# Optimization experiments

Hardware: AMD Instinct MI355X
Metric: run time of the kernel (lower is better)

Reference implementation:

```python
import jax, jax.numpy as jnp
import numpy as np

B, T, N, D = 32, 12, 325, 64
H = 4           # geo_num_heads == t_num_heads
HD = D // H     # head_dim = 16
M_SP = 32       # spatial frequency modes (min(32, N//2))
M_T = T // 2    # temporal frequency modes (all low modes)
SCALE = HD ** -0.5


def _lin(x, W):
    # torch nn.Linear (no bias): y = x @ W.T, W: [out, in]
    return jnp.einsum('btnd,ed->btne', x, W)


def _spatial(x, Wq, Wk, Wv, weights_Q, sp_modes):
    # FEDformer-style frequency attention over the node axis N
    q, k, v = _lin(x, Wq), _lin(x, Wk), _lin(x, Wv)          # [B,T,N,D]
    prep = lambda y: y.reshape(B, T, N, H, HD).transpose(0, 1, 3, 4, 2)  # [B,T,H,HD,N]
    qn = prep(q) / jnp.linalg.norm(q)   # global Frobenius norm (torch.norm with no dim)
    kn = prep(k) / jnp.linalg.norm(k)
    vn = prep(v)
    # rfft over nodes, gather selected modes (scatter-into-zeros in torch == gather here
    # since target indices are 0..M-1)
    qf = jnp.fft.rfft(qn, axis=-1)[..., sp_modes]            # [B,T,H,HD,M] c64
    kf = jnp.fft.rfft(kn, axis=-1)[..., sp_modes]
    vf = jnp.fft.rfft(vn, axis=-1)[..., sp_modes]
    M = M_SP
    qg = qf.transpose(0, 1, 2, 4, 3)[:, :, :, :, None, :]    # [B,T,H,M,1,HD]
    wq = jnp.broadcast_to(weights_Q.astype(jnp.complex64), (B, T, H, M, M - 1, HD))
    q_cat = jnp.concatenate([qg, wq], axis=4)                # [B,T,H,M,M,HD]
    kg = kf.transpose(0, 1, 2, 4, 3)[:, :, :, None, :, :]    # [B,T,H,1,M,HD]
    att = kg * jnp.conj(q_cat) * SCALE                       # [B,T,H,M,M,HD] c64
    att = jax.nn.softmax(jnp.abs(att), axis=-2).astype(jnp.complex64)
    att = att.transpose(0, 1, 2, 3, 5, 4)                    # [B,T,H,M,HD,M]
    vg = vf[:, :, :, None, :, :]                             # [B,T,H,1,HD,M]
    out = (vg * jnp.conj(att)).mean(axis=3)                  # [B,T,H,HD,M]
    out_ft = jnp.zeros((B, T, H, HD, N // 2 + 1), jnp.complex64).at[..., sp_modes].set(out)
    y = jnp.fft.irfft(out_ft, n=N, axis=-1)                  # [B,T,H,HD,N]
    return y.transpose(0, 1, 4, 2, 3).reshape(B, T, N, D)


def _temporal(x, Wq, Wk, Wv, weights_Q_t, t_modes):
    # frequency attention over the time axis T with causal (tril) mask.
    # NOTE: torch reshapes the [B,T,N,D] buffer directly as [B,N,T,H,HD] (raw view),
    # so we replicate that exact buffer reinterpretation.
    q, k, v = _lin(x, Wq), _lin(x, Wk), _lin(x, Wv)
    prep = lambda y: y.reshape(B, N, T, H, HD).transpose(0, 1, 3, 4, 2)  # [B,N,H,HD,T]
    qn = prep(q); kn = prep(k); vn = prep(v)
    qn = qn / jnp.linalg.norm(qn)
    kn = kn / jnp.linalg.norm(kn)
    qf = jnp.fft.rfft(qn, axis=-1)[..., t_modes]             # [B,N,H,HD,Mt]
    kf = jnp.fft.rfft(kn, axis=-1)[..., t_modes]
    vf = jnp.fft.rfft(vn, axis=-1)[..., t_modes]
    Mt = M_T
    qg = qf.transpose(0, 1, 2, 4, 3)[:, :, :, :, None, :]    # [B,N,H,Mt,1,HD]
    wq = jnp.broadcast_to(weights_Q_t.astype(jnp.complex64), (B, N, H, Mt, Mt - 1, HD))
    q_cat = jnp.concatenate([qg, wq], axis=4)                # [B,N,H,Mt,Mt,HD]
    kg = kf.transpose(0, 1, 2, 4, 3)[:, :, :, :, None, :]    # [B,N,H,Mt,1,HD] (unsqueeze(4) in torch)
    att = kg * jnp.conj(q_cat) * SCALE                       # [B,N,H,Mt,Mt,HD]
    att = att.transpose(0, 1, 2, 5, 3, 4)                    # [B,N,H,HD,Mt,Mt]
    mask = jnp.tril(jnp.ones((Mt, Mt), jnp.float32))
    att = att * mask                                         # zero above diagonal
    attw = jax.nn.softmax(jnp.abs(att), axis=-1).astype(jnp.complex64)
    vg = vf[..., None]                                       # [B,N,H,HD,Mt,1]
    out = (vg * jnp.conj(attw)).mean(axis=-1)                # [B,N,H,HD,Mt]
    out_ft = jnp.zeros((B, N, H, HD, T // 2 + 1), jnp.complex64).at[..., t_modes].set(out)
    y = jnp.fft.irfft(out_ft, n=T, axis=-1)                  # [B,N,H,HD,T]
    return y.transpose(0, 4, 1, 2, 3).reshape(B, T, N, D)


def _gcn(x, adj, W_fc1, W_mlp, b_mlp):
    a = adj / jnp.sum(adj, axis=1, keepdims=True)            # row-normalized
    agg = jnp.einsum('btkd,nk->btnd', x, a)
    h = jnp.einsum('btnd,ed->btne', agg, W_fc1)              # fc1 (no bias)
    return jnp.einsum('btnd,ed->btne', h, W_mlp) + b_mlp     # mlp (bias)


def _forward(x, adj, Wq_geo, Wk_geo, Wv_geo, Wq_t, Wk_t, Wv_t,
             W_fc1, W_mlp, b_mlp, weights_Q, weights_Q_t, sp_modes, t_modes):
    gcn_out = _gcn(x, adj, W_fc1, W_mlp, b_mlp)
    sp_x = _spatial(x, Wq_geo, Wk_geo, Wv_geo, weights_Q, sp_modes)
    te_x = _temporal(x, Wq_t, Wk_t, Wv_t, weights_Q_t, t_modes)
    return gcn_out + sp_x + te_x   # proj_drop is identity (p=0)


def setup_inputs() -> dict:
    key = jax.random.key(0)
    ks = jax.random.split(key, 13)
    w = lambda k, s: jax.random.normal(k, s, dtype=jnp.float32) * 0.05
    rng = np.random.default_rng(0)
    sp_modes = np.sort(rng.permutation(N // 2)[:M_SP]).astype(np.int32)
    t_modes = np.arange(M_T, dtype=np.int32)  # modes_T == T//2 selects all low modes
    return {
        'x': jax.random.normal(ks[0], (B, T, N, D), dtype=jnp.float32),
        'adj': jax.random.uniform(ks[1], (N, N), dtype=jnp.float32),
        'Wq_geo': w(ks[2], (D, D)), 'Wk_geo': w(ks[3], (D, D)), 'Wv_geo': w(ks[4], (D, D)),
        'Wq_t': w(ks[5], (D, D)), 'Wk_t': w(ks[6], (D, D)), 'Wv_t': w(ks[7], (D, D)),
        'W_fc1': w(ks[8], (D, D)), 'W_mlp': w(ks[9], (D, D)), 'b_mlp': w(ks[10], (D,)),
        'weights_Q': jax.random.normal(ks[11], (M_SP, M_SP - 1, HD), dtype=jnp.float32),
        'weights_Q_t': jax.random.normal(ks[12], (M_T, M_T - 1, HD), dtype=jnp.float32),
        'sp_modes': jnp.asarray(sp_modes),
        't_modes': jnp.asarray(t_modes),
    }


def reference(x, adj, Wq_geo, Wk_geo, Wv_geo, Wq_t, Wk_t, Wv_t,
              W_fc1, W_mlp, b_mlp, weights_Q, weights_Q_t, sp_modes, t_modes):
    return _forward(x, adj, Wq_geo, Wk_geo, Wv_geo, Wq_t, Wk_t, Wv_t,
                    W_fc1, W_mlp, b_mlp, weights_Q, weights_Q_t, sp_modes, t_modes)
```

## Files before the change

### kernel.cpp

```cpp
#include <hip/hip_runtime.h>


typedef unsigned short u16;
typedef short short8 __attribute__((ext_vector_type(8)));
typedef float floatx4 __attribute__((ext_vector_type(4)));

__device__ __forceinline__ u16 f2bf(float f) {
  union { float fp; unsigned int u; } v; v.fp = f;
  unsigned int x = v.u;
  x += 0x7FFF + ((x >> 16) & 1);
  return (u16)(x >> 16);
}

constexpr size_t OFF_NPART = 4096;
constexpr size_t OFF_WQA  = 8208;
constexpr size_t OFF_ANB  = 24080;
constexpr size_t OFF_TB   = 81280;
constexpr size_t OFF_WVTB = 92544;
constexpr size_t OFF_WBB  = 94592;
constexpr size_t OFF_T2   = 102080;
constexpr size_t OFF_OFT  = 112480;
constexpr size_t OFF_XCT  = 898912;
constexpr size_t OFF_XA   = 13211488;
constexpr size_t OFF_WSPB = OFF_XA + 8192;

__global__ __launch_bounds__(256) void k_prep(const float* __restrict__ adj,
                                              const float* __restrict__ Wmlp,
                                              const float* __restrict__ Wfc1,
                                              const float* __restrict__ wQ,
                                              const float* __restrict__ Wvt,
                                              const float* __restrict__ Wq,
                                              const float* __restrict__ Wk,
                                              const float* __restrict__ Wv,
                                              const int* __restrict__ sp_modes,
                                              float* __restrict__ ws) {
  __shared__ float red[256];
  const int tid = threadIdx.x;
  const int blk = blockIdx.x;
  u16* WBBu = (u16*)(ws + OFF_WBB);
  if (blk == 0) {
    for (int o = tid; o < 4096; o += 256) {
      int g = o >> 6, dd = o & 63;
      float s = 0.f;
      for (int e = 0; e < 64; ++e)
        s = fmaf(Wmlp[g * 64 + e], Wfc1[e * 64 + dd], s);
      WBBu[o] = f2bf(s);
    }
  } else if (blk < 9) {
    for (int i = (blk - 1) * 256 + tid; i < 15872; i += 2048)
      ws[OFF_WQA + i] = fabsf(wQ[i]);
  } else if (blk < 334) {
    const int n = blk - 9;
    float p = 0.f;
    for (int k = tid; k < 325; k += 256) p += adj[n * 325 + k];
    red[tid] = p;
    __syncthreads();
    for (int s2 = 128; s2 > 0; s2 >>= 1) {
      if (tid < s2) red[tid] += red[tid + s2];
      __syncthreads();
    }
    const float inv = 1.f / red[0];
    u16* ANB = (u16*)(ws + OFF_ANB);
    for (int k = tid; k < 352; k += 256)
      ANB[(size_t)n * 352 + k] = (k < 325) ? f2bf(adj[n * 325 + k] * inv) : (u16)0;
  } else if (blk < 366) {
    const int j = blk - 334;
    const int f = sp_modes[j];
    const float wgt = (f == 0) ? 1.f : 2.f;
    u16* T2B = (u16*)(ws + OFF_T2);
    u16* TB = (u16*)(ws + OFF_TB);
    const int row_re = 8 * (j >> 2) + (j & 3);
    const int row_im = row_re + 4;
    for (int n = tid; n < 352; n += 256) {
      float c = 0.f, s = 0.f;
      if (n < 325) {
        int mm = (f * n) % 325;
        float th = 6.283185307179586f * (float)mm * (1.f / 325.f);
        c = cosf(th);
        s = sinf(th);
      }
      TB[(size_t)row_re * 352 + n] = f2bf(c);
      TB[(size_t)row_im * 352 + n] = f2bf(-s);
      if (n < 325) {
        T2B[(size_t)n * 64 + 2 * j] = f2bf(wgt * (1.f / 325.f) * c);
        T2B[(size_t)n * 64 + 2 * j + 1] = f2bf(-wgt * (1.f / 325.f) * s);
      }
    }
  } else if (blk == 366) {
    for (int i = tid; i < 8192; i += 256) {
      const int r = i >> 6, e = i & 63;
      const float* src = (r < 64) ? Wq : Wk;
      WBBu[4096 + i] = f2bf(src[(size_t)(r & 63) * 64 + e]);
    }
  } else if (blk == 367) {
    u16* WSPBu = (u16*)(ws + OFF_WSPB);
    for (int i = tid; i < 12288; i += 256) {
      const int r = i >> 6, e = i & 63;
      const float* src = (r < 64) ? Wq : (r < 128) ? Wk : Wv;
      WSPBu[i] = f2bf(src[(size_t)(r & 63) * 64 + e]);
    }
  } else if (blk == 368) {
    u16* WVTBu = (u16*)(ws + OFF_WVTB);
    for (int i = tid; i < 4096; i += 256) WVTBu[i] = f2bf(Wvt[i]);
  } else {
    const int idx = (blk - 369) * 256 + tid;
    u16* p = (u16*)(ws + OFF_XCT) + (size_t)(idx >> 6) * 22528 + (size_t)(idx & 63) * 352;
    for (int c = 325; c < 352; ++c) p[c] = 0;
  }
}

__global__ __launch_bounds__(512, 3) void k_linear2(const float* __restrict__ x,
                                                    float* __restrict__ ws) {
  __shared__ __align__(16) u16 XA[128 * 72];
  __shared__ float reds[16];
  const int tid = threadIdx.x;
  const int wv = tid >> 6, lane = tid & 63, lc = lane & 15, quad = lane >> 4;
  const size_t base = (size_t)blockIdx.x * 128;
  const u16* WBBu = (const u16*)(ws + OFF_WBB);

  for (int i = tid; i < 2048; i += 512) {
    const int row = i >> 4, e0 = (i & 15) * 4;
    const float4 v = *(const float4*)(x + (base + row) * 64 + e0);
    u16* dst = &XA[row * 72 + e0];
    dst[0] = f2bf(v.x); dst[1] = f2bf(v.y); dst[2] = f2bf(v.z); dst[3] = f2bf(v.w);
  }
  __syncthreads();

  floatx4 acc[12] = {};
#pragma unroll
  for (int kc = 0; kc < 2; ++kc) {
    const short8 af = *(const short8*)&XA[(16 * wv + lc) * 72 + kc * 32 + quad * 8];
#pragma unroll
    for (int ni = 0; ni < 12; ++ni) {
      const short8 bf_ = *(const short8*)&WBBu[(ni * 16 + lc) * 64 + kc * 32 + quad * 8];
      acc[ni] = __builtin_amdgcn_mfma_f32_16x16x32_bf16(af, bf_, acc[ni], 0, 0, 0);
    }
  }

  float sq = 0.f, sk = 0.f;
#pragma unroll
  for (int reg = 0; reg < 4; ++reg) {
#pragma unroll
    for (int ni = 0; ni < 4; ++ni) {
      const float v = acc[4 + ni][reg];
      sq = fmaf(v, v, sq);
    }
#pragma unroll
    for (int ni = 0; ni < 4; ++ni) {
      const float v = acc[8 + ni][reg];
      sk = fmaf(v, v, sk);
    }
  }
  for (int off = 32; off > 0; off >>= 1) {
    sq += __shfl_down(sq, off);
    sk += __shfl_down(sk, off);
  }
  if (lane == 0) { reds[wv] = sq; reds[8 + wv] = sk; }
  __syncthreads();
  if (tid == 0) {
    const float a = reds[0] + reds[1] + reds[2] + reds[3] +
                    reds[4] + reds[5] + reds[6] + reds[7];
    const float b = reds[8] + reds[9] + reds[10] + reds[11] +
                    reds[12] + reds[13] + reds[14] + reds[15];
    *(float2*)(ws + OFF_NPART + 2 * (size_t)blockIdx.x) = make_float2(a, b);
  }

  u16* xcT = XA;
#pragma unroll
  for (int ni = 0; ni < 4; ++ni)
#pragma unroll
    for (int reg = 0; reg < 4; ++reg)
      xcT[(ni * 16 + lc) * 132 + 16 * wv + quad * 4 + reg] = f2bf(acc[ni][reg]);
  __syncthreads();
  u16* XCT = (u16*)(ws + OFF_XCT);
  for (int i = tid; i < 8192; i += 512) {
    const int d = i >> 7, r = i & 127;
    const unsigned int row = (unsigned int)(base + r);
    const unsigned int bt = row / 325u;
    const unsigned int n = row - bt * 325u;
    XCT[(size_t)bt * 22528 + (size_t)d * 352 + n] = xcT[d * 132 + r];
  }
}

__global__ __launch_bounds__(256) void k_spatial3(const float* __restrict__ x,
                                                  float* __restrict__ ws) {
  __shared__ __align__(16) float smem[12816];
  const int tid = threadIdx.x;
  const int bt = blockIdx.x;
  const int lane = tid & 63, wv = tid >> 6;
  const int lc = lane & 15, quad = lane >> 4;
  u16* XBu = (u16*)smem;

  {
    float psq = 0.f, psk = 0.f;
    for (int p = tid; p < 975; p += 256) {
      const float2 v = *(const float2*)(ws + OFF_NPART + 2 * (size_t)p);
      psq += v.x; psk += v.y;
    }
    for (int off = 32; off > 0; off >>= 1) {
      psq += __shfl_down(psq, off);
      psk += __shfl_down(psk, off);
    }
    if (lane == 0) { smem[12800 + wv] = psq; smem[12808 + wv] = psk; }
  }

  const u16* TB = (const u16*)(ws + OFF_TB);
  const u16* WSPBu = (const u16*)(ws + OFF_WSPB);
  const float* xb = x + (size_t)bt * 20800;
  const int br = tid & 31, be0 = (tid >> 5) * 8;

  {
    float va[4][8];
#pragma unroll
    for (int g = 0; g < 3; ++g) {
      const int nkc = (g < 2) ? 4 : 3;
#pragma unroll
      for (int u = 0; u < 4; ++u) {
        if (u >= nkc) break;
        const int k0 = (g * 4 + u) * 32;
        if (k0 + br < 325) {
          const float* src = xb + (size_t)(k0 + br) * 64 + be0;
          *(float4*)&va[u][0] = *(const float4*)src;
          *(float4*)&va[u][4] = *(const float4*)(src + 4);
        } else {
#pragma unroll
          for (int w = 0; w < 8; ++w) va[u][w] = 0.f;
        }
      }
#pragma unroll
      for (int u = 0; u < 4; ++u) {
        if (u >= nkc) break;
        const int k0 = (g * 4 + u) * 32;
#pragma unroll
        for (int w = 0; w < 8; ++w)
          XBu[(be0 + w) * 360 + k0 + br] = f2bf(va[u][w]);
      }
    }
  }
  __syncthreads();

  floatx4 accA[4] = {};
#pragma unroll
  for (int kc = 0; kc < 11; ++kc) {
    const short8 af = *(const short8*)&TB[(size_t)(16 * wv + lc) * 352 + kc * 32 + quad * 8];
#pragma unroll
    for (int t = 0; t < 4; ++t) {
      const short8 bf_ = *(const short8*)&XBu[(t * 16 + lc) * 360 + kc * 32 + quad * 8];
      accA[t] = __builtin_amdgcn_mfma_f32_16x16x32_bf16(af, bf_, accA[t], 0, 0, 0);
    }
  }
  __syncthreads();

  u16* xfl2 = XBu;
#pragma unroll
  for (int t = 0; t < 4; ++t)
#pragma unroll
    for (int r = 0; r < 4; ++r)
      xfl2[(t >> 1) * 2560 + (16 * wv + quad * 4 + r) * 40 + (t & 1) * 16 + lc] =
          f2bf(accA[t][r]);
  __syncthreads();

  floatx4 acc2[12] = {};
#pragma unroll
  for (int kc2 = 0; kc2 < 2; ++kc2) {
    const short8 af2 = *(const short8*)&xfl2[kc2 * 2560 + (16 * wv + lc) * 40 + quad * 8];
#pragma unroll
    for (int t = 0; t < 12; ++t) {
      const short8 bf2 = *(const short8*)&WSPBu[(t * 16 + lc) * 64 + kc2 * 32 + quad * 8];
      acc2[t] = __builtin_amdgcn_mfma_f32_16x16x32_bf16(af2, bf2, acc2[t], 0, 0, 0);
    }
  }
  __syncthreads();

  float* sq_q = smem + 2560;
  float* sq_k = smem + 4608;
  float* vfre = smem + 6656;
  float* vfim = smem + 8704;
  float* wbar = smem + 10752;
  for (int i = tid; i < 2048; i += 256) wbar[i] = 0.f;
  {
    const int fb = 8 * wv + ((quad >= 2) ? 4 : 0);
    const int isim = quad & 1;
#pragma unroll
    for (int t = 0; t < 12; ++t) {
      const int mat = t >> 2;
      const int d = (t & 3) * 16 + lc;
#pragma unroll
      for (int r = 0; r < 4; ++r) {
        const float v = acc2[t][r];
        if (mat == 2) {
          if (isim) vfim[(fb + r) * 64 + d] = v;
          else vfre[(fb + r) * 64 + d] = v;
        } else {
          const float s2 = v * v + __shfl_xor(v * v, 16);
          if (!isim) {
            if (mat == 0) sq_q[(fb + r) * 64 + d] = s2;
            else sq_k[(fb + r) * 64 + d] = s2;
          }
        }
      }
    }
  }
  __syncthreads();
  float nqs = 0.f, nks = 0.f;
#pragma unroll
  for (int w = 0; w < 4; ++w) { nqs += smem[12800 + w]; nks += smem[12808 + w]; }
  const float inv_nq = rsqrtf(nqs);
  const float inv_nk = rsqrtf(nks);
  for (int i = tid; i < 2048; i += 256)
    sq_k[i] = 0.25f * inv_nk * sqrtf(sq_k[i]);
  __syncthreads();
  {
    const int d = tid & 63, fb2 = tid >> 6, hd = d & 15;
    const float* wqa = ws + OFF_WQA;
    float wacc[32];
#pragma unroll
    for (int j = 0; j < 32; ++j) wacc[j] = 0.f;
    for (int r8 = 0; r8 < 8; ++r8) {
      const int m = fb2 + (r8 << 2);
      const float aq = inv_nq * sqrtf(sq_q[m * 64 + d]);
      float sv[32];
      float mx = -1e30f;
#pragma unroll
      for (int j = 0; j < 32; ++j) {
        const float a = (j == 0) ? aq : wqa[(m * 31 + (j - 1)) * 16 + hd];
        const float s = sq_k[j * 64 + d] * a;
        sv[j] = s;
        mx = fmaxf(mx, s);
      }
      float sum = 0.f;
#pragma unroll
      for (int j = 0; j < 32; ++j) {
        const float ev = __expf(sv[j] - mx);
        sv[j] = ev;
        sum += ev;
      }
      const float sc = 0.03125f / sum;
#pragma unroll
      for (int j = 0; j < 32; ++j) wacc[j] += sv[j] * sc;
    }
#pragma unroll
    for (int j = 0; j < 32; ++j) atomicAdd(&wbar[j * 64 + d], wacc[j]);
  }
  __syncthreads();
  unsigned int* OFTu = (unsigned int*)(ws + OFF_OFT) + (size_t)bt * 2048;
  for (int i2 = tid; i2 < 2048; i2 += 256) {
    const int d = i2 >> 5, j = i2 & 31;
    const float w = wbar[j * 64 + d];
    const unsigned int lo = f2bf(vfre[j * 64 + d] * w);
    const unsigned int hi = f2bf(vfim[j * 64 + d] * w);
    OFTu[i2] = lo | (hi << 16);
  }
}

__global__ __launch_bounds__(256) void k_xa(const float* __restrict__ x,
                                            float* __restrict__ ws) {
  const int idx = blockIdx.x * 256 + threadIdx.x;
  if (idx >= 32 * 325 * 16) return;
  const int dq = idx & 15;
  const int n = (idx >> 4) % 325;
  const int b = idx / (16 * 325);
  const float* xp = x + ((size_t)b * 3900 + (size_t)n * 12) * 64 + dq * 4;
  float4 s = make_float4(0.f, 0.f, 0.f, 0.f);
  float sign = 1.f;
  for (int k = 0; k < 12; ++k) {
    const float4 v = *(const float4*)(xp + (size_t)k * 64);
    s.x += sign * v.x; s.y += sign * v.y; s.z += sign * v.z; s.w += sign * v.w;
    sign = -sign;
  }
  *(float4*)(ws + OFF_XA + ((size_t)b * 325 + n) * 64 + dq * 4) = s;
}

__global__ __launch_bounds__(256) void k_final2(const float* __restrict__ x,
                                                const float* __restrict__ bmlp,
                                                float* __restrict__ ws,
                                                float* __restrict__ out) {
  const int tid = threadIdx.x;
  const int bt = blockIdx.x / 3, mc = blockIdx.x % 3;
  const int m0 = mc * 128;
  const int wave = tid >> 6, lane = tid & 63;
  const int quad = lane >> 4, lc = lane & 15;

  const u16* ANB = (const u16*)(ws + OFF_ANB);
  const u16* T2B = (const u16*)(ws + OFF_T2);
  const u16* XCT = (const u16*)(ws + OFF_XCT) + (size_t)bt * 22528;
  const u16* OFT = (const u16*)(ws + OFF_OFT) + (size_t)bt * 4096;
  const u16* WVTBu = (const u16*)(ws + OFF_WVTB);

  const int b = bt / 12, t = bt - b * 12;
  const float sgn12 = ((t & 1) ? -1.f : 1.f) * (1.f / 12.f);

  floatx4 acc[2][4] = {};

#pragma unroll
  for (int c13 = 0; c13 < 13; ++c13) {
    const bool gcn = (c13 < 11);
    const u16* Asrc = gcn ? ANB : T2B;
    const int astr = gcn ? 352 : 64;
    const int acol = gcn ? c13 * 32 : (c13 - 11) * 32;
    const u16* Bsrc = gcn ? XCT : OFT;
    const int bstr = gcn ? 352 : 64;
    short8 af[2], bf_[4];
#pragma unroll
    for (int mi = 0; mi < 2; ++mi) {
      const int gr = m0 + wave * 32 + mi * 16 + lc;
      short8 a = {};
      if (gr < 325)
        a = *(const short8*)&Asrc[(size_t)gr * astr + acol + quad * 8];
      af[mi] = a;
    }
#pragma unroll
    for (int ni = 0; ni < 4; ++ni)
      bf_[ni] = *(const short8*)&Bsrc[(size_t)(ni * 16 + lc) * bstr + acol + quad * 8];
#pragma unroll
    for (int mi = 0; mi < 2; ++mi)
#pragma unroll
      for (int ni = 0; ni < 4; ++ni)
        acc[mi][ni] = __builtin_amdgcn_mfma_f32_16x16x32_bf16(
            af[mi], bf_[ni], acc[mi][ni], 0, 0, 0);
  }

#pragma unroll
  for (int kc = 0; kc < 2; ++kc) {
    const int k0 = kc * 32 + quad * 8;
    short8 af[2];
#pragma unroll
    for (int mi = 0; mi < 2; ++mi) {
      const int nr = m0 + wave * 32 + mi * 16 + lc;
      short8 a = {};
      if (nr < 325) {
        const float* xp = x + ((size_t)b * 3900 + (size_t)nr * 12 + t) * 64 + k0;
        const float* xap = ws + OFF_XA + ((size_t)b * 325 + nr) * 64 + k0;
        float xv[8], av[8];
        *(float4*)xv = *(const float4*)xp;
        *(float4*)(xv + 4) = *(const float4*)(xp + 4);
        *(float4*)av = *(const float4*)xap;
        *(float4*)(av + 4) = *(const float4*)(xap + 4);
#pragma unroll
        for (int u = 0; u < 8; ++u)
          a[u] = (short)f2bf((xv[u] - sgn12 * av[u]) * (1.f / 6.f));
      }
      af[mi] = a;
    }
#pragma unroll
    for (int ni = 0; ni < 4; ++ni) {
      const short8 bf_ = *(const short8*)&WVTBu[(size_t)(ni * 16 + lc) * 64 + k0];
#pragma unroll
      for (int mi = 0; mi < 2; ++mi)
        acc[mi][ni] = __builtin_amdgcn_mfma_f32_16x16x32_bf16(
            af[mi], bf_, acc[mi][ni], 0, 0, 0);
    }
  }

#pragma unroll
  for (int ni = 0; ni < 4; ++ni) {
    const int d = ni * 16 + lc;
    const float bias = bmlp[d];
#pragma unroll
    for (int mi = 0; mi < 2; ++mi) {
#pragma unroll
      for (int reg = 0; reg < 4; ++reg) {
        const int n = m0 + wave * 32 + mi * 16 + quad * 4 + reg;
        if (n >= 325) continue;
        out[((size_t)bt * 325 + n) * 64 + d] = acc[mi][ni][reg] + bias;
      }
    }
  }
}

extern "C" void kernel_launch(void* const* d_in, const int* in_sizes, int n_in,
                              void* d_out, int out_size, void* d_ws, size_t ws_size,
                              hipStream_t stream) {
  const float* x = (const float*)d_in[0];
  const float* adj = (const float*)d_in[1];
  const float* Wq_g = (const float*)d_in[2];
  const float* Wk_g = (const float*)d_in[3];
  const float* Wv_g = (const float*)d_in[4];
  const float* Wv_t = (const float*)d_in[7];
  const float* Wfc1 = (const float*)d_in[8];
  const float* Wmlp = (const float*)d_in[9];
  const float* bmlp = (const float*)d_in[10];
  const float* wQ = (const float*)d_in[11];
  const int* sp_modes = (const int*)d_in[13];
  float* ws = (float*)d_ws;
  float* out = (float*)d_out;

  (void)in_sizes; (void)n_in; (void)out_size; (void)ws_size;

  k_prep<<<465, 256, 0, stream>>>(adj, Wmlp, Wfc1, wQ, Wv_t, Wq_g, Wk_g, Wv_g,
                                  sp_modes, ws);
  k_linear2<<<975, 512, 0, stream>>>(x, ws);
  k_spatial3<<<384, 256, 0, stream>>>(x, ws);
  k_xa<<<650, 256, 0, stream>>>(x, ws);
  k_final2<<<1152, 256, 0, stream>>>(x, bmlp, ws, out);
}
```

Baseline: 253.9 us.

## Fuse linear, spatial and alternating-sum kernels into one launch; move norm partials to prep

Splits the old k_linear2 into two parts. The q/k norm-partial GEMM now runs in extra k_prep blocks, converting Wq/Wk to bf16 inline, so the norms are ready before the spatial stage. The remaining x@Wcomb projection, the spatial frequency attention and the alternating-sum over time are merged into one k_mega launch, partitioned by block index. This cuts the pipeline from five launches to three and lets independent work share the GPU. The price is that the q/k projection is recomputed and the workspace layout is reshuffled.

```diff
diff --git a/kernel.cpp b/kernel.cpp
--- a/kernel.cpp
+++ b/kernel.cpp
@@ -16,15 +16,16 @@
 constexpr size_t OFF_WQA  = 8208;
 constexpr size_t OFF_ANB  = 24080;
 constexpr size_t OFF_TB   = 81280;
-constexpr size_t OFF_WVTB = 92544;
-constexpr size_t OFF_WBB  = 94592;
 constexpr size_t OFF_T2   = 102080;
 constexpr size_t OFF_OFT  = 112480;
 constexpr size_t OFF_XCT  = 898912;
+constexpr size_t OFF_WBB  = 5224288;
+constexpr size_t OFF_WSPB = 5226336;
+constexpr size_t OFF_WVTB = 5232480;
 constexpr size_t OFF_XA   = 13211488;
-constexpr size_t OFF_WSPB = OFF_XA + 8192;
-
-__global__ __launch_bounds__(256) void k_prep(const float* __restrict__ adj,
+
+__global__ __launch_bounds__(256) void k_prep(const float* __restrict__ x,
+                                              const float* __restrict__ adj,
                                               const float* __restrict__ Wmlp,
                                               const float* __restrict__ Wfc1,
                                               const float* __restrict__ wQ,
@@ -35,9 +36,72 @@
                                               const int* __restrict__ sp_modes,
                                               float* __restrict__ ws) {
   __shared__ float red[256];
+  __shared__ __align__(16) u16 XA[128 * 72];
   const int tid = threadIdx.x;
   const int blk = blockIdx.x;
   u16* WBBu = (u16*)(ws + OFF_WBB);
+  if (blk >= 464) {
+    const int blk2 = blk - 464;
+    const int wv = tid >> 6, lane = tid & 63, lc = lane & 15, quad = lane >> 4;
+    const size_t base = (size_t)blk2 * 128;
+    for (int i = tid; i < 2048; i += 256) {
+      const int row = i >> 4, e0 = (i & 15) * 4;
+      const float4 v = *(const float4*)(x + (base + row) * 64 + e0);
+      u16* dst = &XA[row * 72 + e0];
+      dst[0] = f2bf(v.x); dst[1] = f2bf(v.y); dst[2] = f2bf(v.z); dst[3] = f2bf(v.w);
+    }
+    __syncthreads();
+    floatx4 acc[2][8] = {};
+#pragma unroll
+    for (int kc = 0; kc < 2; ++kc) {
+      short8 af[2];
+#pragma unroll
+      for (int mi = 0; mi < 2; ++mi)
+        af[mi] = *(const short8*)&XA[(32 * wv + 16 * mi + lc) * 72 + kc * 32 + quad * 8];
+#pragma unroll
+      for (int ni = 0; ni < 8; ++ni) {
+        const int g = (ni & 3) * 16 + lc;
+        const float* src = ((ni < 4) ? Wq : Wk) + (size_t)g * 64 + kc * 32 + quad * 8;
+        float v8[8];
+        *(float4*)v8 = *(const float4*)src;
+        *(float4*)(v8 + 4) = *(const float4*)(src + 4);
+        short8 bf_;
+#pragma unroll
+        for (int u = 0; u < 8; ++u) bf_[u] = (short)f2bf(v8[u]);
+#pragma unroll
+        for (int mi = 0; mi < 2; ++mi)
+          acc[mi][ni] = __builtin_amdgcn_mfma_f32_16x16x32_bf16(af[mi], bf_, acc[mi][ni], 0, 0, 0);
+      }
+    }
+    float sq = 0.f, sk = 0.f;
+#pragma unroll
+    for (int mi = 0; mi < 2; ++mi)
+#pragma unroll
+      for (int reg = 0; reg < 4; ++reg) {
+#pragma unroll
+        for (int ni = 0; ni < 4; ++ni) {
+          const float v = acc[mi][ni][reg];
+          sq = fmaf(v, v, sq);
+        }
+#pragma unroll
+        for (int ni = 4; ni < 8; ++ni) {
+          const float v = acc[mi][ni][reg];
+          sk = fmaf(v, v, sk);
+        }
+      }
+    for (int off = 32; off > 0; off >>= 1) {
+      sq += __shfl_down(sq, off);
+      sk += __shfl_down(sk, off);
+    }
+    if (lane == 0) { red[wv] = sq; red[8 + wv] = sk; }
+    __syncthreads();
+    if (tid == 0) {
+      const float a = red[0] + red[1] + red[2] + red[3];
+      const float b = red[8] + red[9] + red[10] + red[11];
+      *(float2*)(ws + OFF_NPART + 2 * (size_t)blk2) = make_float2(a, b);
+    }
+    return;
+  }
   if (blk == 0) {
     for (int o = tid; o < 4096; o += 256) {
       int g = o >> 6, dd = o & 63;
@@ -87,288 +151,259 @@
       }
     }
   } else if (blk == 366) {
-    for (int i = tid; i < 8192; i += 256) {
-      const int r = i >> 6, e = i & 63;
-      const float* src = (r < 64) ? Wq : Wk;
-      WBBu[4096 + i] = f2bf(src[(size_t)(r & 63) * 64 + e]);
-    }
-  } else if (blk == 367) {
     u16* WSPBu = (u16*)(ws + OFF_WSPB);
     for (int i = tid; i < 12288; i += 256) {
       const int r = i >> 6, e = i & 63;
       const float* src = (r < 64) ? Wq : (r < 128) ? Wk : Wv;
       WSPBu[i] = f2bf(src[(size_t)(r & 63) * 64 + e]);
     }
-  } else if (blk == 368) {
+  } else if (blk == 367) {
     u16* WVTBu = (u16*)(ws + OFF_WVTB);
     for (int i = tid; i < 4096; i += 256) WVTBu[i] = f2bf(Wvt[i]);
   } else {
-    const int idx = (blk - 369) * 256 + tid;
+    const int idx = (blk - 368) * 256 + tid;
     u16* p = (u16*)(ws + OFF_XCT) + (size_t)(idx >> 6) * 22528 + (size_t)(idx & 63) * 352;
     for (int c = 325; c < 352; ++c) p[c] = 0;
   }
 }
 
-__global__ __launch_bounds__(512, 3) void k_linear2(const float* __restrict__ x,
-                                                    float* __restrict__ ws) {
-  __shared__ __align__(16) u16 XA[128 * 72];
-  __shared__ float reds[16];
-  const int tid = threadIdx.x;
-  const int wv = tid >> 6, lane = tid & 63, lc = lane & 15, quad = lane >> 4;
-  const size_t base = (size_t)blockIdx.x * 128;
-  const u16* WBBu = (const u16*)(ws + OFF_WBB);
-
-  for (int i = tid; i < 2048; i += 512) {
-    const int row = i >> 4, e0 = (i & 15) * 4;
-    const float4 v = *(const float4*)(x + (base + row) * 64 + e0);
-    u16* dst = &XA[row * 72 + e0];
-    dst[0] = f2bf(v.x); dst[1] = f2bf(v.y); dst[2] = f2bf(v.z); dst[3] = f2bf(v.w);
-  }
-  __syncthreads();
-
-  floatx4 acc[12] = {};
-#pragma unroll
-  for (int kc = 0; kc < 2; ++kc) {
-    const short8 af = *(const short8*)&XA[(16 * wv + lc) * 72 + kc * 32 + quad * 8];
-#pragma unroll
-    for (int ni = 0; ni < 12; ++ni) {
-      const short8 bf_ = *(const short8*)&WBBu[(ni * 16 + lc) * 64 + kc * 32 + quad * 8];
-      acc[ni] = __builtin_amdgcn_mfma_f32_16x16x32_bf16(af, bf_, acc[ni], 0, 0, 0);
-    }
-  }
-
-  float sq = 0.f, sk = 0.f;
-#pragma unroll
-  for (int reg = 0; reg < 4; ++reg) {
-#pragma unroll
-    for (int ni = 0; ni < 4; ++ni) {
-      const float v = acc[4 + ni][reg];
-      sq = fmaf(v, v, sq);
-    }
-#pragma unroll
-    for (int ni = 0; ni < 4; ++ni) {
-      const float v = acc[8 + ni][reg];
-      sk = fmaf(v, v, sk);
-    }
-  }
-  for (int off = 32; off > 0; off >>= 1) {
-    sq += __shfl_down(sq, off);
-    sk += __shfl_down(sk, off);
-  }
-  if (lane == 0) { reds[wv] = sq; reds[8 + wv] = sk; }
-  __syncthreads();
-  if (tid == 0) {
-    const float a = reds[0] + reds[1] + reds[2] + reds[3] +
-                    reds[4] + reds[5] + reds[6] + reds[7];
-    const float b = reds[8] + reds[9] + reds[10] + reds[11] +
-                    reds[12] + reds[13] + reds[14] + reds[15];
-    *(float2*)(ws + OFF_NPART + 2 * (size_t)blockIdx.x) = make_float2(a, b);
-  }
-
-  u16* xcT = XA;
-#pragma unroll
-  for (int ni = 0; ni < 4; ++ni)
-#pragma unroll
-    for (int reg = 0; reg < 4; ++reg)
-      xcT[(ni * 16 + lc) * 132 + 16 * wv + quad * 4 + reg] = f2bf(acc[ni][reg]);
-  __syncthreads();
-  u16* XCT = (u16*)(ws + OFF_XCT);
-  for (int i = tid; i < 8192; i += 512) {
-    const int d = i >> 7, r = i & 127;
-    const unsigned int row = (unsigned int)(base + r);
-    const unsigned int bt = row / 325u;
-    const unsigned int n = row - bt * 325u;
-    XCT[(size_t)bt * 22528 + (size_t)d * 352 + n] = xcT[d * 132 + r];
-  }
-}
-
-__global__ __launch_bounds__(256) void k_spatial3(const float* __restrict__ x,
-                                                  float* __restrict__ ws) {
+__global__ __launch_bounds__(256) void k_mega(const float* __restrict__ x,
+                                              float* __restrict__ ws) {
   __shared__ __align__(16) float smem[12816];
   const int tid = threadIdx.x;
-  const int bt = blockIdx.x;
+  const int blk = blockIdx.x;
   const int lane = tid & 63, wv = tid >> 6;
   const int lc = lane & 15, quad = lane >> 4;
-  u16* XBu = (u16*)smem;
-
-  {
-    float psq = 0.f, psk = 0.f;
-    for (int p = tid; p < 975; p += 256) {
-      const float2 v = *(const float2*)(ws + OFF_NPART + 2 * (size_t)p);
-      psq += v.x; psk += v.y;
-    }
-    for (int off = 32; off > 0; off >>= 1) {
-      psq += __shfl_down(psq, off);
-      psk += __shfl_down(psk, off);
-    }
-    if (lane == 0) { smem[12800 + wv] = psq; smem[12808 + wv] = psk; }
+
+  if (blk < 384) {
+    const int bt = blk;
+    u16* XBu = (u16*)smem;
+
+    {
+      float psq = 0.f, psk = 0.f;
+      for (int p = tid; p < 975; p += 256) {
+        const float2 v = *(const float2*)(ws + OFF_NPART + 2 * (size_t)p);
+        psq += v.x; psk += v.y;
+      }
+      for (int off = 32; off > 0; off >>= 1) {
+        psq += __shfl_down(psq, off);
+        psk += __shfl_down(psk, off);
+      }
+      if (lane == 0) { smem[12800 + wv] = psq; smem[12808 + wv] = psk; }
+    }
+
+    const u16* TB = (const u16*)(ws + OFF_TB);
+    const u16* WSPBu = (const u16*)(ws + OFF_WSPB);
+    const float* xb = x + (size_t)bt * 20800;
+    const int br = tid & 31, be0 = (tid >> 5) * 8;
+
+    {
+      float va[4][8];
+#pragma unroll
+      for (int g = 0; g < 3; ++g) {
+        const int nkc = (g < 2) ? 4 : 3;
+#pragma unroll
+        for (int u = 0; u < 4; ++u) {
+          if (u >= nkc) break;
+          const int k0 = (g * 4 + u) * 32;
+          if (k0 + br < 325) {
+            const float* src = xb + (size_t)(k0 + br) * 64 + be0;
+            *(float4*)&va[u][0] = *(const float4*)src;
+            *(float4*)&va[u][4] = *(const float4*)(src + 4);
+          } else {
+#pragma unroll
+            for (int w = 0; w < 8; ++w) va[u][w] = 0.f;
+          }
+        }
+#pragma unroll
+        for (int u = 0; u < 4; ++u) {
+          if (u >= nkc) break;
+          const int k0 = (g * 4 + u) * 32;
+#pragma unroll
+          for (int w = 0; w < 8; ++w)
+            XBu[(be0 + w) * 360 + k0 + br] = f2bf(va[u][w]);
+        }
+      }
+    }
+    __syncthreads();
+
+    floatx4 accA[4] = {};
+#pragma unroll
+    for (int kc = 0; kc < 11; ++kc) {
+      const short8 af = *(const short8*)&TB[(size_t)(16 * wv + lc) * 352 + kc * 32 + quad * 8];
+#pragma unroll
+      for (int t = 0; t < 4; ++t) {
+        const short8 bf_ = *(const short8*)&XBu[(t * 16 + lc) * 360 + kc * 32 + quad * 8];
+        accA[t] = __builtin_amdgcn_mfma_f32_16x16x32_bf16(af, bf_, accA[t], 0, 0, 0);
+      }
+    }
+    __syncthreads();
+
+    u16* xfl2 = XBu;
+#pragma unroll
+    for (int t = 0; t < 4; ++t)
+#pragma unroll
+      for (int r = 0; r < 4; ++r)
+        xfl2[(t >> 1) * 2560 + (16 * wv + quad * 4 + r) * 40 + (t & 1) * 16 + lc] =
+            f2bf(accA[t][r]);
+    __syncthreads();
+
+    floatx4 acc2[12] = {};
+#pragma unroll
+    for (int kc2 = 0; kc2 < 2; ++kc2) {
+      const short8 af2 = *(const short8*)&xfl2[kc2 * 2560 + (16 * wv + lc) * 40 + quad * 8];
+#pragma unroll
+      for (int t = 0; t < 12; ++t) {
+        const short8 bf2 = *(const short8*)&WSPBu[(t * 16 + lc) * 64 + kc2 * 32 + quad * 8];
+        acc2[t] = __builtin_amdgcn_mfma_f32_16x16x32_bf16(af2, bf2, acc2[t], 0, 0, 0);
+      }
+    }
+    __syncthreads();
+
+    float* sq_q = smem + 2560;
+    float* sq_k = smem + 4608;
+    float* vfre = smem + 6656;
+    float* vfim = smem + 8704;
+    float* wbar = smem + 10752;
+    for (int i = tid; i < 2048; i += 256) wbar[i] = 0.f;
+    {
+      const int fb = 8 * wv + ((quad >= 2) ? 4 : 0);
+      const int isim = quad & 1;
+#pragma unroll
+      for (int t = 0; t < 12; ++t) {
+        const int mat = t >> 2;
+        const int d = (t & 3) * 16 + lc;
+#pragma unroll
+        for (int r = 0; r < 4; ++r) {
+          const float v = acc2[t][r];
+          if (mat == 2) {
+            if (isim) vfim[(fb + r) * 64 + d] = v;
+            else vfre[(fb + r) * 64 + d] = v;
+          } else {
+            const float s2 = v * v + __shfl_xor(v * v, 16);
+            if (!isim) {
+              if (mat == 0) sq_q[(fb + r) * 64 + d] = s2;
+              else sq_k[(fb + r) * 64 + d] = s2;
+            }
+          }
+        }
+      }
+    }
+    __syncthreads();
+    float nqs = 0.f, nks = 0.f;
+#pragma unroll
+    for (int w = 0; w < 4; ++w) { nqs += smem[12800 + w]; nks += smem[12808 + w]; }
+    const float inv_nq = rsqrtf(nqs);
+    const float inv_nk = rsqrtf(nks);
+    for (int i = tid; i < 2048; i += 256)
+      sq_k[i] = 0.25f * inv_nk * sqrtf(sq_k[i]);
+    __syncthreads();
+    {
+      const int d = tid & 63, fb2 = tid >> 6, hd = d & 15;
+      const float* wqa = ws + OFF_WQA;
+      float wacc[32];
+#pragma unroll
+      for (int j = 0; j < 32; ++j) wacc[j] = 0.f;
+      for (int r8 = 0; r8 < 8; ++r8) {
+        const int m = fb2 + (r8 << 2);
+        const float aq = inv_nq * sqrtf(sq_q[m * 64 + d]);
+        float sv[32];
+        float mx = -1e30f;
+#pragma unroll
+        for (int j = 0; j < 32; ++j) {
+          const float a = (j == 0) ? aq : wqa[(m * 31 + (j - 1)) * 16 + hd];
+          const float s = sq_k[j * 64 + d] * a;
+          sv[j] = s;
+          mx = fmaxf(mx, s);
+        }
+        float sum = 0.f;
+#pragma unroll
+        for (int j = 0; j < 32; ++j) {
+          const float ev = __expf(sv[j] - mx);
+          sv[j] = ev;
+          sum += ev;
+        }
+        const float sc = 0.03125f / sum;
+#pragma unroll
+        for (int j = 0; j < 32; ++j) wacc[j] += sv[j] * sc;
+      }
+#pragma unroll
+      for (int j = 0; j < 32; ++j) atomicAdd(&wbar[j * 64 + d], wacc[j]);
+    }
+    __syncthreads();
+    unsigned int* OFTu = (unsigned int*)(ws + OFF_OFT) + (size_t)bt * 2048;
+    for (int i2 = tid; i2 < 2048; i2 += 256) {
+      const int d = i2 >> 5, j = i2 & 31;
+      const float w = wbar[j * 64 + d];
+      const unsigned int lo = f2bf(vfre[j * 64 + d] * w);
+      const unsigned int hi = f2bf(vfim[j * 64 + d] * w);
+      OFTu[i2] = lo | (hi << 16);
+    }
+  } else if (blk < 1359) {
+    const int blk2 = blk - 384;
+    u16* XAu = (u16*)smem;
+    const size_t base = (size_t)blk2 * 128;
+    const u16* WBBu = (const u16*)(ws + OFF_WBB);
+
+    for (int i = tid; i < 2048; i += 256) {
+      const int row = i >> 4, e0 = (i & 15) * 4;
+      const float4 v = *(const float4*)(x + (base + row) * 64 + e0);
+      u16* dst = &XAu[row * 72 + e0];
+      dst[0] = f2bf(v.x); dst[1] = f2bf(v.y); dst[2] = f2bf(v.z); dst[3] = f2bf(v.w);
+    }
+    __syncthreads();
+
+    floatx4 acc[2][4] = {};
+#pragma unroll
+    for (int kc = 0; kc < 2; ++kc) {
+      short8 af[2];
+#pragma unroll
+      for (int mi = 0; mi < 2; ++mi)
+        af[mi] = *(const short8*)&XAu[(32 * wv + 16 * mi + lc) * 72 + kc * 32 + quad * 8];
+#pragma unroll
+      for (int ni = 0; ni < 4; ++ni) {
+        const short8 bf_ = *(const short8*)&WBBu[(ni * 16 + lc) * 64 + kc * 32 + quad * 8];
+#pragma unroll
+        for (int mi = 0; mi < 2; ++mi)
+          acc[mi][ni] = __builtin_amdgcn_mfma_f32_16x16x32_bf16(af[mi], bf_, acc[mi][ni], 0, 0, 0);
+      }
+    }
+    __syncthreads();
+
+    u16* xcT = XAu;
+#pragma unroll
+    for (int ni = 0; ni < 4; ++ni)
+#pragma unroll
+      for (int mi = 0; mi < 2; ++mi)
+#pragma unroll
+        for (int reg = 0; reg < 4; ++reg)
+          xcT[(ni * 16 + lc) * 132 + 32 * wv + 16 * mi + quad * 4 + reg] =
+              f2bf(acc[mi][ni][reg]);
+    __syncthreads();
+    u16* XCT = (u16*)(ws + OFF_XCT);
+    for (int i = tid; i < 8192; i += 256) {
+      const int d = i >> 7, r = i & 127;
+      const unsigned int row = (unsigned int)(base + r);
+      const unsigned int bt = row / 325u;
+      const unsigned int n = row - bt * 325u;
+      XCT[(size_t)bt * 22528 + (size_t)d * 352 + n] = xcT[d * 132 + r];
+    }
+  } else {
+    const int idx = (blk - 1359) * 256 + tid;
+    if (idx >= 32 * 325 * 16) return;
+    const int dq = idx & 15;
+    const int n = (idx >> 4) % 325;
+    const int b = idx / (16 * 325);
+    const float* xp = x + ((size_t)b * 3900 + (size_t)n * 12) * 64 + dq * 4;
+    float4 s = make_float4(0.f, 0.f, 0.f, 0.f);
+    float sign = 1.f;
+    for (int k = 0; k < 12; ++k) {
+      const float4 v = *(const float4*)(xp + (size_t)k * 64);
+      s.x += sign * v.x; s.y += sign * v.y; s.z += sign * v.z; s.w += sign * v.w;
+      sign = -sign;
+    }
+    *(float4*)(ws + OFF_XA + ((size_t)b * 325 + n) * 64 + dq * 4) = s;
   }
-
-  const u16* TB = (const u16*)(ws + OFF_TB);
-  const u16* WSPBu = (const u16*)(ws + OFF_WSPB);
-  const float* xb = x + (size_t)bt * 20800;
-  const int br = tid & 31, be0 = (tid >> 5) * 8;
-
-  {
-    float va[4][8];
-#pragma unroll
-    for (int g = 0; g < 3; ++g) {
-      const int nkc = (g < 2) ? 4 : 3;
-#pragma unroll
-      for (int u = 0; u < 4; ++u) {
-        if (u >= nkc) break;
-        const int k0 = (g * 4 + u) * 32;
-        if (k0 + br < 325) {
-          const float* src = xb + (size_t)(k0 + br) * 64 + be0;
-          *(float4*)&va[u][0] = *(const float4*)src;
-          *(float4*)&va[u][4] = *(const float4*)(src + 4);
-        } else {
-#pragma unroll
-          for (int w = 0; w < 8; ++w) va[u][w] = 0.f;
-        }
-      }
-#pragma unroll
-      for (int u = 0; u < 4; ++u) {
-        if (u >= nkc) break;
-        const int k0 = (g * 4 + u) * 32;
-#pragma unroll
-        for (int w = 0; w < 8; ++w)
-          XBu[(be0 + w) * 360 + k0 + br] = f2bf(va[u][w]);
-      }
-    }
-  }
-  __syncthreads();
-
-  floatx4 accA[4] = {};
-#pragma unroll
-  for (int kc = 0; kc < 11; ++kc) {
-    const short8 af = *(const short8*)&TB[(size_t)(16 * wv + lc) * 352 + kc * 32 + quad * 8];
-#pragma unroll
-    for (int t = 0; t < 4; ++t) {
-      const short8 bf_ = *(const short8*)&XBu[(t * 16 + lc) * 360 + kc * 32 + quad * 8];
-      accA[t] = __builtin_amdgcn_mfma_f32_16x16x32_bf16(af, bf_, accA[t], 0, 0, 0);
-    }
-  }
-  __syncthreads();
-
-  u16* xfl2 = XBu;
-#pragma unroll
-  for (int t = 0; t < 4; ++t)
-#pragma unroll
-    for (int r = 0; r < 4; ++r)
-      xfl2[(t >> 1) * 2560 + (16 * wv + quad * 4 + r) * 40 + (t & 1) * 16 + lc] =
-          f2bf(accA[t][r]);
-  __syncthreads();
-
-  floatx4 acc2[12] = {};
-#pragma unroll
-  for (int kc2 = 0; kc2 < 2; ++kc2) {
-    const short8 af2 = *(const short8*)&xfl2[kc2 * 2560 + (16 * wv + lc) * 40 + quad * 8];
-#pragma unroll
-    for (int t = 0; t < 12; ++t) {
-      const short8 bf2 = *(const short8*)&WSPBu[(t * 16 + lc) * 64 + kc2 * 32 + quad * 8];
-      acc2[t] = __builtin_amdgcn_mfma_f32_16x16x32_bf16(af2, bf2, acc2[t], 0, 0, 0);
-    }
-  }
-  __syncthreads();
-
-  float* sq_q = smem + 2560;
-  float* sq_k = smem + 4608;
-  float* vfre = smem + 6656;
-  float* vfim = smem + 8704;
-  float* wbar = smem + 10752;
-  for (int i = tid; i < 2048; i += 256) wbar[i] = 0.f;
-  {
-    const int fb = 8 * wv + ((quad >= 2) ? 4 : 0);
-    const int isim = quad & 1;
-#pragma unroll
-    for (int t = 0; t < 12; ++t) {
-      const int mat = t >> 2;
-      const int d = (t & 3) * 16 + lc;
-#pragma unroll
-      for (int r = 0; r < 4; ++r) {
-        const float v = acc2[t][r];
-        if (mat == 2) {
-          if (isim) vfim[(fb + r) * 64 + d] = v;
-          else vfre[(fb + r) * 64 + d] = v;
-        } else {
-          const float s2 = v * v + __shfl_xor(v * v, 16);
-          if (!isim) {
-            if (mat == 0) sq_q[(fb + r) * 64 + d] = s2;
-            else sq_k[(fb + r) * 64 + d] = s2;
-          }
-        }
-      }
-    }
-  }
-  __syncthreads();
-  float nqs = 0.f, nks = 0.f;
-#pragma unroll
-  for (int w = 0; w < 4; ++w) { nqs += smem[12800 + w]; nks += smem[12808 + w]; }
-  const float inv_nq = rsqrtf(nqs);
-  const float inv_nk = rsqrtf(nks);
-  for (int i = tid; i < 2048; i += 256)
-    sq_k[i] = 0.25f * inv_nk * sqrtf(sq_k[i]);
-  __syncthreads();
-  {
-    const int d = tid & 63, fb2 = tid >> 6, hd = d & 15;
-    const float* wqa = ws + OFF_WQA;
-    float wacc[32];
-#pragma unroll
-    for (int j = 0; j < 32; ++j) wacc[j] = 0.f;
-    for (int r8 = 0; r8 < 8; ++r8) {
-      const int m = fb2 + (r8 << 2);
-      const float aq = inv_nq * sqrtf(sq_q[m * 64 + d]);
-      float sv[32];
-      float mx = -1e30f;
-#pragma unroll
-      for (int j = 0; j < 32; ++j) {
-        const float a = (j == 0) ? aq : wqa[(m * 31 + (j - 1)) * 16 + hd];
-        const float s = sq_k[j * 64 + d] * a;
-        sv[j] = s;
-        mx = fmaxf(mx, s);
-      }
-      float sum = 0.f;
-#pragma unroll
-      for (int j = 0; j < 32; ++j) {
-        const float ev = __expf(sv[j] - mx);
-        sv[j] = ev;
-        sum += ev;
-      }
-      const float sc = 0.03125f / sum;
-#pragma unroll
-      for (int j = 0; j < 32; ++j) wacc[j] += sv[j] * sc;
-    }
-#pragma unroll
-    for (int j = 0; j < 32; ++j) atomicAdd(&wbar[j * 64 + d], wacc[j]);
-  }
-  __syncthreads();
-  unsigned int* OFTu = (unsigned int*)(ws + OFF_OFT) + (size_t)bt * 2048;
-  for (int i2 = tid; i2 < 2048; i2 += 256) {
-    const int d = i2 >> 5, j = i2 & 31;
-    const float w = wbar[j * 64 + d];
-    const unsigned int lo = f2bf(vfre[j * 64 + d] * w);
-    const unsigned int hi = f2bf(vfim[j * 64 + d] * w);
-    OFTu[i2] = lo | (hi << 16);
-  }
-}
-
-__global__ __launch_bounds__(256) void k_xa(const float* __restrict__ x,
-                                            float* __restrict__ ws) {
-  const int idx = blockIdx.x * 256 + threadIdx.x;
-  if (idx >= 32 * 325 * 16) return;
-  const int dq = idx & 15;
-  const int n = (idx >> 4) % 325;
-  const int b = idx / (16 * 325);
-  const float* xp = x + ((size_t)b * 3900 + (size_t)n * 12) * 64 + dq * 4;
-  float4 s = make_float4(0.f, 0.f, 0.f, 0.f);
-  float sign = 1.f;
-  for (int k = 0; k < 12; ++k) {
-    const float4 v = *(const float4*)(xp + (size_t)k * 64);
-    s.x += sign * v.x; s.y += sign * v.y; s.z += sign * v.z; s.w += sign * v.w;
-    sign = -sign;
-  }
-  *(float4*)(ws + OFF_XA + ((size_t)b * 325 + n) * 64 + dq * 4) = s;
 }
 
 __global__ __launch_bounds__(256) void k_final2(const float* __restrict__ x,
@@ -487,10 +522,8 @@
 
   (void)in_sizes; (void)n_in; (void)out_size; (void)ws_size;
 
-  k_prep<<<465, 256, 0, stream>>>(adj, Wmlp, Wfc1, wQ, Wv_t, Wq_g, Wk_g, Wv_g,
-                                  sp_modes, ws);
-  k_linear2<<<975, 512, 0, stream>>>(x, ws);
-  k_spatial3<<<384, 256, 0, stream>>>(x, ws);
-  k_xa<<<650, 256, 0, stream>>>(x, ws);
+  k_prep<<<1439, 256, 0, stream>>>(x, adj, Wmlp, Wfc1, wQ, Wv_t, Wq_g, Wk_g, Wv_g,
+                                   sp_modes, ws);
+  k_mega<<<2009, 256, 0, stream>>>(x, ws);
   k_final2<<<1152, 256, 0, stream>>>(x, bmlp, ws, out);
 }
```

After: 233.7 us. 7.9% less time.
